# Kernel optimization log

Measured on AMD Instinct MI355X. Metric: run time of the kernel, lower is better.

## Reference

```python
import jax, jax.numpy as jnp
import numpy as np

N, C, CS, H = 2048, 768, 384, 16
D = C // H  # 48, per-head dim


def _ln(x, eps=1e-5):
    # torch LayerNorm: population variance over last dim
    m = jnp.mean(x, axis=-1, keepdims=True)
    v = jnp.var(x, axis=-1, keepdims=True)
    return (x - m) * jax.lax.rsqrt(v + eps)


def setup_inputs() -> dict:
    key = jax.random.key(0)
    ks = jax.random.split(key, 12)
    s = 0.02  # small init scale for weights
    return {
        "x": jax.random.normal(ks[0], (N, C), jnp.float32),
        "mask": jnp.ones((N,), jnp.float32),
        "pair_logits": jax.random.normal(ks[1], (H, N, N), jnp.float32),
        "single_cond": jax.random.normal(ks[2], (N, CS), jnp.float32),
        "q_w": jax.random.normal(ks[3], (C, C), jnp.float32) * s,
        "q_b": jnp.zeros((C,), jnp.float32),
        "k_w": jax.random.normal(ks[4], (C, C), jnp.float32) * s,
        "v_w": jax.random.normal(ks[5], (C, C), jnp.float32) * s,
        "gate_w": jax.random.normal(ks[6], (C, C), jnp.float32) * s,
        "sc_ln_w": jnp.ones((CS,), jnp.float32),
        "scale_w": jax.random.normal(ks[7], (C, CS), jnp.float32) * s,
        "scale_b": jnp.zeros((C,), jnp.float32),
        "bias_w": jax.random.normal(ks[8], (C, CS), jnp.float32) * s,
        "t2_w": jax.random.normal(ks[9], (C, C), jnp.float32) * s,
        "az_w": jax.random.normal(ks[10], (C, CS), jnp.float32) * s,
        "az_b": jnp.zeros((C,), jnp.float32),
    }


def reference(x, mask, pair_logits, single_cond, q_w, q_b, k_w, v_w, gate_w,
              sc_ln_w, scale_w, scale_b, bias_w, t2_w, az_w, az_b):
    n = x.shape[0]
    mask_bias = (1e9 * (mask - 1.0))[None, None, :]  # (1,1,N) additive bias
    # AdaptiveLayerNorm (use_single_cond=True)
    xn = _ln(x)                                      # no affine
    sc = _ln(single_cond) * sc_ln_w                  # LN with weight, no bias
    xm = jax.nn.sigmoid(sc @ scale_w.T + scale_b) * xn + sc @ bias_w.T
    # qkv projections -> (n, h, d)
    q = (xm @ q_w.T + q_b).reshape(n, H, D)
    k = (xm @ k_w.T).reshape(n, H, D)
    v = (xm @ v_w.T).reshape(n, H, D)
    logits = jnp.einsum('qhc,khc->hqk', q * (D ** -0.5), k) + mask_bias
    logits = logits + pair_logits
    weights = jax.nn.softmax(logits, axis=-1)        # (h, n, n)
    wavg = jnp.einsum('hqk,khc->qhc', weights, v).reshape(n, C)
    wavg = wavg * jax.nn.sigmoid(xm @ gate_w.T)      # sigmoid gating
    # AdaLNZero
    out = wavg @ t2_w.T
    out = jax.nn.sigmoid(single_cond @ az_w.T + az_b) * out
    return out
```

## Files before the change

kernel.cpp:

```cpp
#include <hip/hip_runtime.h>

typedef unsigned short u16;
typedef __attribute__((ext_vector_type(8))) short short8;
typedef __attribute__((ext_vector_type(4))) float f32x4;
typedef __attribute__((ext_vector_type(4))) unsigned short us4;

#define MFMA(a,b,c) __builtin_amdgcn_mfma_f32_16x16x32_bf16(a,b,c,0,0,0)
#define LOG2E 1.44269504088896341f
#define FENCE asm volatile("" ::: "memory")

__device__ __forceinline__ u16 f2bf(float f) {
  unsigned u = __builtin_bit_cast(unsigned, f);
  return (u16)((u + 0x7FFFu + ((u >> 16) & 1u)) >> 16);
}
__device__ __forceinline__ float bf2f(u16 u) {
  return __builtin_bit_cast(float, (unsigned)u << 16);
}
__device__ __forceinline__ unsigned cvtpk(float a, float b) {
  unsigned r;
  asm("v_cvt_pk_bf16_f32 %0, %1, %2" : "=v"(r) : "v"(a), "v"(b));
  return r;
}
__device__ __forceinline__ float sigmoidf_(float x) { return 1.f / (1.f + __expf(-x)); }

__device__ __forceinline__ void gload16(const void* g, void* l) {
  __builtin_amdgcn_global_load_lds(
      (const __attribute__((address_space(1))) void*)g,
      (__attribute__((address_space(3))) void*)l, 16, 0, 0);
}

__global__ __launch_bounds__(256) void cvt_weights(
    const float* __restrict__ sw, const float* __restrict__ bw, const float* __restrict__ aw,
    const float* __restrict__ qw, const float* __restrict__ kw, const float* __restrict__ vw,
    const float* __restrict__ gw, const float* __restrict__ tw,
    u16* __restrict__ wsb, u16* __restrict__ waz, u16* __restrict__ wqkvg, u16* __restrict__ wt2)
{
  long i = ((long)blockIdx.x * 256 + threadIdx.x) * 4;
  const float* src; u16* dst;
  if      (i < 294912)  { src = sw + i;             dst = wsb + i; }
  else if (i < 589824)  { src = bw + (i - 294912);  dst = wsb + i; }
  else if (i < 884736)  { src = aw + (i - 589824);  dst = waz + (i - 589824); }
  else if (i < 1474560) { src = qw + (i - 884736);  dst = wqkvg + (i - 884736); }
  else if (i < 2064384) { src = kw + (i - 1474560); dst = wqkvg + (i - 884736); }
  else if (i < 2654208) { src = vw + (i - 2064384); dst = wqkvg + (i - 884736); }
  else if (i < 3244032) { src = gw + (i - 2654208); dst = wqkvg + (i - 884736); }
  else                  { src = tw + (i - 3244032); dst = wt2 + (i - 3244032); }
  f32x4 v = *(const f32x4*)src;
  us4 o = { f2bf(v[0]), f2bf(v[1]), f2bf(v[2]), f2bf(v[3]) };
  *(us4*)dst = o;
}

__device__ __forceinline__ void blockreduce2(float& a, float& b) {
  #pragma unroll
  for (int d = 1; d < 64; d <<= 1) { a += __shfl_xor(a, d); b += __shfl_xor(b, d); }
  __shared__ float red[8];
  int w = threadIdx.x >> 6, l = threadIdx.x & 63;
  if (l == 0) { red[w] = a; red[4 + w] = b; }
  __syncthreads();
  a = red[0] + red[1] + red[2] + red[3];
  b = red[4] + red[5] + red[6] + red[7];
}

__global__ __launch_bounds__(256) void ln_prep(
    const float* __restrict__ x, const float* __restrict__ sc,
    const float* __restrict__ sc_ln_w, const float* __restrict__ mask,
    float* __restrict__ xn, u16* __restrict__ sc_bf, u16* __restrict__ scr_bf,
    float* __restrict__ mbv)
{
  int bid = blockIdx.x, t = threadIdx.x;
  if (bid < 2048) {
    const float* row = x + (long)bid * 768;
    float v0 = row[t], v1 = row[t + 256], v2 = row[t + 512];
    float s = v0 + v1 + v2, sq = v0*v0 + v1*v1 + v2*v2;
    blockreduce2(s, sq);
    float mean = s * (1.f / 768.f);
    float var = sq * (1.f / 768.f) - mean * mean;
    float rs = rsqrtf(var + 1e-5f);
    float* orow = xn + (long)bid * 768;
    orow[t] = (v0 - mean) * rs; orow[t + 256] = (v1 - mean) * rs; orow[t + 512] = (v2 - mean) * rs;
  } else if (bid < 4096) {
    int r = bid - 2048;
    const float* row = sc + (long)r * 384;
    float v0 = row[t];
    float v1 = (t < 128) ? row[t + 256] : 0.f;
    float s = v0 + v1, sq = v0*v0 + v1*v1;
    blockreduce2(s, sq);
    float mean = s * (1.f / 384.f), var = sq * (1.f / 384.f) - mean * mean;
    float rs = rsqrtf(var + 1e-5f);
    sc_bf[r*384 + t]  = f2bf((v0 - mean) * rs * sc_ln_w[t]);
    scr_bf[r*384 + t] = f2bf(v0);
    if (t < 128) {
      sc_bf[r*384 + t + 256]  = f2bf((v1 - mean) * rs * sc_ln_w[t + 256]);
      scr_bf[r*384 + t + 256] = f2bf(v1);
    }
  } else {
    for (int i = t; i < 2048; i += 256) mbv[i] = 1e9f * (mask[i] - 1.f);
  }
}

__global__ __launch_bounds__(256) void gemm_bf16_64(
    const u16* __restrict__ X, const u16* __restrict__ W,
    float* __restrict__ Y, int M, int K)
{
  __shared__ u16 lA[2048];
  __shared__ u16 lB[2048];
  const int row0 = blockIdx.x << 6;
  const int col0 = blockIdx.y << 6;
  const int tid = threadIdx.x;
  const int w = tid >> 6, l = tid & 63;
  const int wr = (w >> 1) << 5, wc = (w & 1) << 5;
  const int g = l >> 4, r16 = l & 15;
  const int srow = w * 16 + (l >> 2);
  const int scol = (l & 3) * 8;
  f32x4 acc[2][2] = {};
  for (int k0 = 0; k0 < K; k0 += 32) {
    gload16(X + (long)(row0 + srow) * K + k0 + scol, &lA[w*512]);
    gload16(W + (long)(col0 + srow) * K + k0 + scol, &lB[w*512]);
    __syncthreads();
    short8 af[2], bw_[2];
    #pragma unroll
    for (int i = 0; i < 2; ++i) { af[i]  = *(const short8*)&lA[(wr + i*16 + r16)*32 + g*8]; }
    #pragma unroll
    for (int j = 0; j < 2; ++j) { bw_[j] = *(const short8*)&lB[(wc + j*16 + r16)*32 + g*8]; }
    #pragma unroll
    for (int i = 0; i < 2; ++i)
      #pragma unroll
      for (int j = 0; j < 2; ++j)
        acc[i][j] = MFMA(af[i], bw_[j], acc[i][j]);
    __syncthreads();
  }
  #pragma unroll
  for (int i = 0; i < 2; ++i) {
    #pragma unroll
    for (int j = 0; j < 2; ++j) {
      long rr = row0 + wr + i*16 + g*4;
      int cc = col0 + wc + j*16 + r16;
      #pragma unroll
      for (int r = 0; r < 4; ++r) { Y[(rr + r) * M + cc] = acc[i][j][r]; }
    }
  }
}

__global__ __launch_bounds__(256) void gemm_az64(
    const u16* __restrict__ X, const u16* __restrict__ W,
    const float* __restrict__ azs, float* __restrict__ Y, int M, int K)
{
  __shared__ u16 lA[2048];
  __shared__ u16 lB[2048];
  const int row0 = blockIdx.x << 6;
  const int col0 = blockIdx.y << 6;
  const int tid = threadIdx.x;
  const int w = tid >> 6, l = tid & 63;
  const int wr = (w >> 1) << 5, wc = (w & 1) << 5;
  const int g = l >> 4, r16 = l & 15;
  const int srow = w * 16 + (l >> 2);
  const int scol = (l & 3) * 8;
  f32x4 acc[2][2] = {};
  for (int k0 = 0; k0 < K; k0 += 32) {
    gload16(X + (long)(row0 + srow) * K + k0 + scol, &lA[w*512]);
    gload16(W + (long)(col0 + srow) * K + k0 + scol, &lB[w*512]);
    __syncthreads();
    short8 af[2], bw_[2];
    #pragma unroll
    for (int i = 0; i < 2; ++i) { af[i]  = *(const short8*)&lA[(wr + i*16 + r16)*32 + g*8]; }
    #pragma unroll
    for (int j = 0; j < 2; ++j) { bw_[j] = *(const short8*)&lB[(wc + j*16 + r16)*32 + g*8]; }
    #pragma unroll
    for (int i = 0; i < 2; ++i)
      #pragma unroll
      for (int j = 0; j < 2; ++j)
        acc[i][j] = MFMA(af[i], bw_[j], acc[i][j]);
    __syncthreads();
  }
  #pragma unroll
  for (int i = 0; i < 2; ++i) {
    #pragma unroll
    for (int j = 0; j < 2; ++j) {
      long rr = row0 + wr + i*16 + g*4;
      int cc = col0 + wc + j*16 + r16;
      #pragma unroll
      for (int r = 0; r < 4; ++r) {
        Y[(rr + r) * M + cc] = acc[i][j][r] * azs[(rr + r) * M + cc];
      }
    }
  }
}

__global__ __launch_bounds__(256) void gemm_qkvg64(
    const u16* __restrict__ X, const u16* __restrict__ W,
    const float* __restrict__ q_b,
    u16* __restrict__ qpad, u16* __restrict__ kpad,
    u16* __restrict__ vt, u16* __restrict__ gsig)
{
  __shared__ u16 lA[2048];
  __shared__ u16 lB[2048];
  const int K = 768;
  const int row0 = blockIdx.x << 6;
  const int col0 = blockIdx.y << 6;
  const int tid = threadIdx.x;
  const int w = tid >> 6, l = tid & 63;
  const int wr = (w >> 1) << 5, wc = (w & 1) << 5;
  const int g = l >> 4, r16 = l & 15;
  const int srow = w * 16 + (l >> 2);
  const int scol = (l & 3) * 8;
  f32x4 acc[2][2] = {};
  for (int k0 = 0; k0 < K; k0 += 32) {
    gload16(X + (long)(row0 + srow) * K + k0 + scol, &lA[w*512]);
    gload16(W + (long)(col0 + srow) * K + k0 + scol, &lB[w*512]);
    __syncthreads();
    short8 af[2], bw_[2];
    #pragma unroll
    for (int i = 0; i < 2; ++i) { af[i]  = *(const short8*)&lA[(wr + i*16 + r16)*32 + g*8]; }
    #pragma unroll
    for (int j = 0; j < 2; ++j) { bw_[j] = *(const short8*)&lB[(wc + j*16 + r16)*32 + g*8]; }
    #pragma unroll
    for (int i = 0; i < 2; ++i)
      #pragma unroll
      for (int j = 0; j < 2; ++j)
        acc[i][j] = MFMA(af[i], bw_[j], acc[i][j]);
    __syncthreads();
  }
  const int sec = (col0 >= 2304) ? 3 : (col0 >= 1536) ? 2 : (col0 >= 768) ? 1 : 0;
  #pragma unroll
  for (int i = 0; i < 2; ++i) {
    #pragma unroll
    for (int j = 0; j < 2; ++j) {
      int rr = row0 + wr + i*16 + g*4;
      int cc = col0 + wc + j*16 + r16;
      if (sec == 0) {
        int m = cc, h = m / 48, d = m - h * 48;
        float qb = q_b[m];
        #pragma unroll
        for (int r = 0; r < 4; ++r)
          qpad[((long)h*2048 + rr + r)*64 + d] =
              f2bf((acc[i][j][r] + qb) * 0.14433756729740643f);
      } else if (sec == 1) {
        int m = cc - 768, h = m / 48, d = m - h * 48;
        #pragma unroll
        for (int r = 0; r < 4; ++r)
          kpad[((long)h*2048 + rr + r)*64 + d] = f2bf(acc[i][j][r]);
      } else if (sec == 2) {
        int m = cc - 1536, h = m / 48, d = m - h * 48;
        us4 o = { f2bf(acc[i][j][0]), f2bf(acc[i][j][1]),
                  f2bf(acc[i][j][2]), f2bf(acc[i][j][3]) };
        *(us4*)(vt + ((long)h*48 + d)*2048 + rr) = o;
      } else {
        int m = cc - 2304;
        #pragma unroll
        for (int r = 0; r < 4; ++r)
          gsig[(long)(rr + r)*768 + m] = f2bf(sigmoidf_(acc[i][j][r]));
      }
    }
  }
}

__global__ __launch_bounds__(256) void pad_init(
    const float* __restrict__ mbv, u16* __restrict__ qpad, u16* __restrict__ kpad)
{
  int t = blockIdx.x * 256 + threadIdx.x;
  int n = t & 2047;
  long base = (long)t * 64 + 48;
  us4 z = {0, 0, 0, 0};
  us4 q0 = { f2bf(1.0f), 0, 0, 0 };
  us4 k0 = { f2bf(mbv[n]), 0, 0, 0 };
  *(us4*)(qpad + base) = q0;  *(us4*)(qpad + base + 4) = z;
  *(us4*)(qpad + base + 8) = z; *(us4*)(qpad + base + 12) = z;
  *(us4*)(kpad + base) = k0;  *(us4*)(kpad + base + 4) = z;
  *(us4*)(kpad + base + 8) = z; *(us4*)(kpad + base + 12) = z;
}

__global__ __launch_bounds__(256) void ada_kernel(
    const float* __restrict__ Y1, const float* __restrict__ Yaz,
    const float* __restrict__ xn, const float* __restrict__ scale_b,
    const float* __restrict__ az_b, u16* __restrict__ xm, float* __restrict__ azsig)
{
  long e = ((long)blockIdx.x * 256 + threadIdx.x) * 4;
  int n = (int)(e / 768), c = (int)(e % 768);
  f32x4 ys = *(const f32x4*)(Y1 + (long)n*1536 + c);
  f32x4 yb = *(const f32x4*)(Y1 + (long)n*1536 + 768 + c);
  f32x4 xv = *(const f32x4*)(xn + e);
  f32x4 sb = *(const f32x4*)(scale_b + c);
  f32x4 ya = *(const f32x4*)(Yaz + e);
  f32x4 ab = *(const f32x4*)(az_b + c);
  us4 o; f32x4 az;
  #pragma unroll
  for (int k = 0; k < 4; ++k) {
    o[k] = f2bf(sigmoidf_(ys[k] + sb[k]) * xv[k] + yb[k]);
    az[k] = sigmoidf_(ya[k] + ab[k]);
  }
  *(us4*)(xm + e) = o;
  *(f32x4*)(azsig + e) = az;
}

__global__ __launch_bounds__(256, 3) void attn_kernel(
    const u16* __restrict__ qpad, const u16* __restrict__ kpad,
    const u16* __restrict__ vt, const float* __restrict__ pair,
    const u16* __restrict__ gsig, u16* __restrict__ wg)
{
  __shared__ __align__(16) char smem[36864];
  const int bid = blockIdx.x;
  const int h = ((bid & 7) << 1) | ((bid >> 3) & 1);
  const int qb = bid >> 4;
  const int tid = threadIdx.x, w = tid >> 6, l = tid & 63;
  const int g = l >> 4, q = l & 15;
  const int qrow = qb * 64 + w * 16 + q;

  const u16* qbase = qpad + ((long)h * 2048 + qrow) * 64;
  short8 qf0 = *(const short8*)(qbase + g * 8);
  short8 qf1 = *(const short8*)(qbase + 32 + g * 8);

  const float* prow = pair + ((long)h * 2048 + qrow) * 2048;
  const u16*   kgl  = kpad + (long)h * 2048 * 64;
  const u16*   vgl  = vt   + (long)h * 48 * 2048;
  const int sr8 = l >> 3, sc8 = l & 7;
  unsigned* pl = (unsigned*)(smem + 28672) + w*512 + q*32;
  const int sx = (q & 7) << 2;

  f32x4 prA[4], prB[4];

  #define STAGE_PR(KT, BUF) do {                                                  \
    _Pragma("unroll")                                                             \
    for (int mf_ = 0; mf_ < 4; ++mf_)                                             \
      BUF[mf_] = __builtin_nontemporal_load(                                      \
          (const f32x4*)(prow + (long)(KT)*64 + mf_*16 + g*4));                   \
  } while (0)

  #define STAGE_KV(KT, BI) do {                                                   \
    char* kd = smem + (BI)*8192 + w*2048;                                          \
    _Pragma("unroll")                                                              \
    for (int i_ = 0; i_ < 2; ++i_) {                                               \
      int row_ = i_*8 + sr8;                                                       \
      gload16(kgl + (long)((KT)*64 + w*16 + row_)*64 + ((sc8 ^ (row_&7)) << 3),    \
              kd + i_*1024);                                                       \
    }                                                                              \
    if (w > 0) {                                                                   \
      char* vd = smem + 16384 + (BI)*6144 + (w-1)*2048;                            \
      _Pragma("unroll")                                                            \
      for (int i_ = 0; i_ < 2; ++i_) {                                             \
        int row_ = i_*8 + sr8;                                                     \
        gload16(vgl + (long)((w-1)*16 + row_)*2048 + (KT)*64 +                     \
                ((sc8 ^ (row_&7)) << 3), vd + i_*1024);                            \
      }                                                                            \
    }                                                                              \
  } while (0)

  STAGE_PR(0, prA); STAGE_KV(0, 0);
  STAGE_PR(1, prB); STAGE_KV(1, 1);

  float m = -1e30f, ssum = 0.f;
  f32x4 o0 = {0,0,0,0}, o1 = {0,0,0,0}, o2 = {0,0,0,0};

  #define BODY(T, PRBUF, PAR) do {                                                \
    if ((T) == 31)   { asm volatile("s_waitcnt vmcnt(0)" ::: "memory"); }          \
    else if (w == 0) { asm volatile("s_waitcnt vmcnt(6)" ::: "memory"); }          \
    else             { asm volatile("s_waitcnt vmcnt(8)" ::: "memory"); }          \
    __builtin_amdgcn_s_barrier();                                                  \
    FENCE;                                                                         \
    const char* kb = smem + (PAR)*8192;                                            \
    const char* vb = smem + 16384 + (PAR)*6144;                                    \
    f32x4 s[4];                                                                    \
    _Pragma("unroll")                                                              \
    for (int mf = 0; mf < 4; ++mf) {                                               \
      const int kr = mf*16 + q;                                                    \
      short8 ka = *(const short8*)(kb + kr*128 + ((g       ^ (q&7)) << 4));        \
      short8 kc = *(const short8*)(kb + kr*128 + (((g + 4) ^ (q&7)) << 4));        \
      s[mf] = MFMA(ka, qf0, PRBUF[mf]);                                            \
      s[mf] = MFMA(kc, qf1, s[mf]);                                                \
    }                                                                              \
    float tmax = -3e38f;                                                           \
    _Pragma("unroll")                                                              \
    for (int mf = 0; mf < 4; ++mf)                                                 \
      tmax = fmaxf(tmax, fmaxf(fmaxf(s[mf][0], s[mf][1]), fmaxf(s[mf][2], s[mf][3])));\
    tmax = fmaxf(tmax, __shfl_xor(tmax, 16));                                      \
    tmax = fmaxf(tmax, __shfl_xor(tmax, 32));                                      \
    float mnew = fmaxf(m, tmax);                                                   \
    float alpha = exp2f((m - mnew) * LOG2E);                                       \
    m = mnew;                                                                      \
    float mL = mnew * LOG2E;                                                       \
    float psum = 0.f;                                                              \
    unsigned pk0[4], pk1[4];                                                       \
    _Pragma("unroll")                                                              \
    for (int mf = 0; mf < 4; ++mf) {                                               \
      float p0 = exp2f(fmaf(s[mf][0], LOG2E, -mL));                                \
      float p1 = exp2f(fmaf(s[mf][1], LOG2E, -mL));                                \
      float p2 = exp2f(fmaf(s[mf][2], LOG2E, -mL));                                \
      float p3 = exp2f(fmaf(s[mf][3], LOG2E, -mL));                                \
      psum += (p0 + p1) + (p2 + p3);                                               \
      pk0[mf] = cvtpk(p0, p1);                                                     \
      pk1[mf] = cvtpk(p2, p3);                                                     \
    }                                                                              \
    ssum = ssum * alpha + psum;                                                    \
    o0 *= alpha; o1 *= alpha; o2 *= alpha;                                         \
    _Pragma("unroll")                                                              \
    for (int mf = 0; mf < 4; ++mf) {                                               \
      uint2 pv_; pv_.x = pk0[mf]; pv_.y = pk1[mf];                                 \
      *(uint2*)(pl + ((mf*8 + g*2) ^ sx)) = pv_;                                   \
    }                                                                              \
    asm volatile("s_waitcnt lgkmcnt(0)" ::: "memory");                             \
    __builtin_amdgcn_sched_barrier(0);                                             \
    _Pragma("unroll")                                                              \
    for (int ks = 0; ks < 2; ++ks) {                                               \
      union { uint4 u4; short8 v; } pf;                                            \
      pf.u4 = *(const uint4*)(pl + ((ks*16 + g*4) ^ sx));                          \
      const int vc = ((ks*4 + g) ^ (q & 7)) << 4;                                  \
      short8 v0 = *(const short8*)(vb + (q)*128      + vc);                        \
      short8 v1 = *(const short8*)(vb + (16 + q)*128 + vc);                        \
      short8 v2 = *(const short8*)(vb + (32 + q)*128 + vc);                        \
      o0 = MFMA(v0, pf.v, o0);                                                     \
      o1 = MFMA(v1, pf.v, o1);                                                     \
      o2 = MFMA(v2, pf.v, o2);                                                     \
    }                                                                              \
    FENCE;                                                                         \
    __builtin_amdgcn_s_barrier();                                                  \
    FENCE;                                                                         \
    if ((T) < 30) { STAGE_PR((T)+2, PRBUF); STAGE_KV((T)+2, PAR); }                \
    __builtin_amdgcn_sched_barrier(0);                                             \
  } while (0)

  for (int t = 0; t < 32; t += 2) {
    BODY(t,     prA, 0);
    BODY(t + 1, prB, 1);
  }
  #undef BODY
  #undef STAGE_PR
  #undef STAGE_KV

  ssum += __shfl_xor(ssum, 16);
  ssum += __shfl_xor(ssum, 32);
  float rinv = 1.f / ssum;
  const long nbase = (long)qrow * 768 + h * 48;
  #pragma unroll
  for (int r = 0; r < 3; ++r) {
    f32x4 ov = (r == 0) ? o0 : ((r == 1) ? o1 : o2);
    int c = r * 16 + g * 4;
    us4 gs = *(const us4*)(gsig + nbase + c);
    us4 ou;
    #pragma unroll
    for (int j = 0; j < 4; ++j) ou[j] = f2bf(ov[j] * rinv * bf2f(gs[j]));
    *(us4*)(wg + nbase + c) = ou;
  }
}

extern "C" void kernel_launch(void* const* d_in, const int* in_sizes, int n_in,
                              void* d_out, int out_size, void* d_ws, size_t ws_size,
                              hipStream_t stream) {
  const float* x       = (const float*)d_in[0];
  const float* mask    = (const float*)d_in[1];
  const float* pair    = (const float*)d_in[2];
  const float* sc      = (const float*)d_in[3];
  const float* q_w     = (const float*)d_in[4];
  const float* q_b     = (const float*)d_in[5];
  const float* k_w     = (const float*)d_in[6];
  const float* v_w     = (const float*)d_in[7];
  const float* g_w     = (const float*)d_in[8];
  const float* slw     = (const float*)d_in[9];
  const float* scale_w = (const float*)d_in[10];
  const float* scale_b = (const float*)d_in[11];
  const float* bias_w  = (const float*)d_in[12];
  const float* t2_w    = (const float*)d_in[13];
  const float* az_w    = (const float*)d_in[14];
  const float* az_b    = (const float*)d_in[15];
  float* out = (float*)d_out;
  char* ws = (char*)d_ws;

  u16*   Wsb   = (u16*)  (ws + 0);
  u16*   Waz   = (u16*)  (ws + 1179648);
  u16*   Wqkvg = (u16*)  (ws + 1769472);
  u16*   Wt2   = (u16*)  (ws + 6488064);
  float* xn    = (float*)(ws + 7667712);
  u16*   sc_bf = (u16*)  (ws + 13959168);
  u16*   scr_bf= (u16*)  (ws + 15532032);
  u16*   wg    = (u16*)  (ws + 13959168);
  float* mb    = (float*)(ws + 17104896);
  float* Y1    = (float*)(ws + 17113088);
  u16*   qpad  = (u16*)  (ws + 17113088);
  u16*   kpad  = (u16*)  (ws + 21307392);
  float* Yaz   = (float*)(ws + 29696000);
  u16*   xm    = (u16*)  (ws + 35987456);
  float* azsig = (float*)(ws + 39133184);
  u16*   vt    = (u16*)  (ws + 70590464);
  u16*   gsig  = (u16*)  (ws + 73736192);

  cvt_weights<<<3744, 256, 0, stream>>>(scale_w, bias_w, az_w, q_w, k_w, v_w, g_w, t2_w,
                                        Wsb, Waz, Wqkvg, Wt2);
  ln_prep<<<4097, 256, 0, stream>>>(x, sc, slw, mask, xn, sc_bf, scr_bf, mb);
  gemm_bf16_64<<<dim3(32, 24), 256, 0, stream>>>(sc_bf, Wsb, Y1, 1536, 384);
  gemm_bf16_64<<<dim3(32, 12), 256, 0, stream>>>(scr_bf, Waz, Yaz, 768, 384);
  ada_kernel<<<1536, 256, 0, stream>>>(Y1, Yaz, xn, scale_b, az_b, xm, azsig);
  gemm_qkvg64<<<dim3(32, 48), 256, 0, stream>>>(xm, Wqkvg, q_b, qpad, kpad, vt, gsig);
  pad_init<<<128, 256, 0, stream>>>(mb, qpad, kpad);
  attn_kernel<<<512, 256, 0, stream>>>(qpad, kpad, vt, pair, gsig, wg);
  gemm_az64<<<dim3(32, 12), 256, 0, stream>>>(wg, Wt2, azsig, out, 768, 768);
}
```

Baseline: 164.0 us.

## Split attention over two key halves with a separate combine kernel

Splits the attention kernel along the key dimension into two halves (split-K / flash-decoding style). The grid doubles from 512 to 1024 blocks, and each block writes unnormalized partial outputs plus its running max and sum to workspace. A new combine kernel rescales the two partials, normalizes, applies the sigmoid gate and writes bf16 output. This targets low occupancy, since 512 blocks at 3 per CU underfill 256 CUs. The cost is extra fp32 partial traffic, one more launch, and a shorter pipelined loop per block.

```diff
diff --git a/kernel.cpp b/kernel.cpp
--- a/kernel.cpp
+++ b/kernel.cpp
@@ -292,15 +292,16 @@
   *(f32x4*)(azsig + e) = az;
 }
 
-__global__ __launch_bounds__(256, 3) void attn_kernel(
+__global__ __launch_bounds__(256, 3) void attn_partial(
     const u16* __restrict__ qpad, const u16* __restrict__ kpad,
     const u16* __restrict__ vt, const float* __restrict__ pair,
-    const u16* __restrict__ gsig, u16* __restrict__ wg)
+    float* __restrict__ po, float* __restrict__ pms)
 {
   __shared__ __align__(16) char smem[36864];
   const int bid = blockIdx.x;
   const int h = ((bid & 7) << 1) | ((bid >> 3) & 1);
-  const int qb = bid >> 4;
+  const int kh = (bid >> 4) & 1;
+  const int qb = bid >> 5;
   const int tid = threadIdx.x, w = tid >> 6, l = tid & 63;
   const int g = l >> 4, q = l & 15;
   const int qrow = qb * 64 + w * 16 + q;
@@ -309,9 +310,9 @@
   short8 qf0 = *(const short8*)(qbase + g * 8);
   short8 qf1 = *(const short8*)(qbase + 32 + g * 8);
 
-  const float* prow = pair + ((long)h * 2048 + qrow) * 2048;
-  const u16*   kgl  = kpad + (long)h * 2048 * 64;
-  const u16*   vgl  = vt   + (long)h * 48 * 2048;
+  const float* prow = pair + ((long)h * 2048 + qrow) * 2048 + kh * 1024;
+  const u16*   kgl  = kpad + (long)h * 2048 * 64 + (long)kh * 1024 * 64;
+  const u16*   vgl  = vt   + (long)h * 48 * 2048 + kh * 1024;
   const int sr8 = l >> 3, sc8 = l & 7;
   unsigned* pl = (unsigned*)(smem + 28672) + w*512 + q*32;
   const int sx = (q & 7) << 2;
@@ -351,7 +352,7 @@
   f32x4 o0 = {0,0,0,0}, o1 = {0,0,0,0}, o2 = {0,0,0,0};
 
   #define BODY(T, PRBUF, PAR) do {                                                \
-    if ((T) == 31)   { asm volatile("s_waitcnt vmcnt(0)" ::: "memory"); }          \
+    if ((T) == 15)   { asm volatile("s_waitcnt vmcnt(0)" ::: "memory"); }          \
     else if (w == 0) { asm volatile("s_waitcnt vmcnt(6)" ::: "memory"); }          \
     else             { asm volatile("s_waitcnt vmcnt(8)" ::: "memory"); }          \
     __builtin_amdgcn_s_barrier();                                                  \
@@ -413,11 +414,11 @@
     FENCE;                                                                         \
     __builtin_amdgcn_s_barrier();                                                  \
     FENCE;                                                                         \
-    if ((T) < 30) { STAGE_PR((T)+2, PRBUF); STAGE_KV((T)+2, PAR); }                \
+    if ((T) < 14) { STAGE_PR((T)+2, PRBUF); STAGE_KV((T)+2, PAR); }                \
     __builtin_amdgcn_sched_barrier(0);                                             \
   } while (0)
 
-  for (int t = 0; t < 32; t += 2) {
+  for (int t = 0; t < 16; t += 2) {
     BODY(t,     prA, 0);
     BODY(t + 1, prB, 1);
   }
@@ -427,18 +428,35 @@
 
   ssum += __shfl_xor(ssum, 16);
   ssum += __shfl_xor(ssum, 32);
-  float rinv = 1.f / ssum;
-  const long nbase = (long)qrow * 768 + h * 48;
+  if (g == 0) {
+    *(float2*)(pms + ((long)(kh*16 + h)*2048 + qrow)*2) = make_float2(m, ssum);
+  }
+  const long pbase = (long)kh*1572864 + (long)qrow*768 + h*48;
+  *(f32x4*)(po + pbase + g*4)      = o0;
+  *(f32x4*)(po + pbase + 16 + g*4) = o1;
+  *(f32x4*)(po + pbase + 32 + g*4) = o2;
+}
+
+__global__ __launch_bounds__(256) void attn_combine(
+    const float* __restrict__ po, const float* __restrict__ pms,
+    const u16* __restrict__ gsig, u16* __restrict__ wg)
+{
+  long e = ((long)blockIdx.x * 256 + threadIdx.x) * 4;
+  int n = (int)(e / 768), c = (int)(e % 768), h = c / 48;
+  f32x4 a0 = *(const f32x4*)(po + e);
+  f32x4 a1 = *(const f32x4*)(po + 1572864 + e);
+  float2 p0 = *(const float2*)(pms + ((long)h*2048 + n)*2);
+  float2 p1 = *(const float2*)(pms + ((long)(16+h)*2048 + n)*2);
+  float M = fmaxf(p0.x, p1.x);
+  float e0 = exp2f((p0.x - M) * LOG2E);
+  float e1 = exp2f((p1.x - M) * LOG2E);
+  float rinv = 1.f / (p0.y * e0 + p1.y * e1);
+  us4 gs = *(const us4*)(gsig + e);
+  us4 ou;
   #pragma unroll
-  for (int r = 0; r < 3; ++r) {
-    f32x4 ov = (r == 0) ? o0 : ((r == 1) ? o1 : o2);
-    int c = r * 16 + g * 4;
-    us4 gs = *(const us4*)(gsig + nbase + c);
-    us4 ou;
-    #pragma unroll
-    for (int j = 0; j < 4; ++j) ou[j] = f2bf(ov[j] * rinv * bf2f(gs[j]));
-    *(us4*)(wg + nbase + c) = ou;
-  }
+  for (int j = 0; j < 4; ++j)
+    ou[j] = f2bf((a0[j]*e0 + a1[j]*e1) * rinv * bf2f(gs[j]));
+  *(us4*)(wg + e) = ou;
 }
 
 extern "C" void kernel_launch(void* const* d_in, const int* in_sizes, int n_in,
@@ -478,6 +496,8 @@
   float* Yaz   = (float*)(ws + 29696000);
   u16*   xm    = (u16*)  (ws + 35987456);
   float* azsig = (float*)(ws + 39133184);
+  float* po    = (float*)(ws + 45424640);
+  float* pms   = (float*)(ws + 58007552);
   u16*   vt    = (u16*)  (ws + 70590464);
   u16*   gsig  = (u16*)  (ws + 73736192);
 
@@ -489,6 +509,7 @@
   ada_kernel<<<1536, 256, 0, stream>>>(Y1, Yaz, xn, scale_b, az_b, xm, azsig);
   gemm_qkvg64<<<dim3(32, 48), 256, 0, stream>>>(xm, Wqkvg, q_b, qpad, kpad, vt, gsig);
   pad_init<<<128, 256, 0, stream>>>(mb, qpad, kpad);
-  attn_kernel<<<512, 256, 0, stream>>>(qpad, kpad, vt, pair, gsig, wg);
+  attn_partial<<<1024, 256, 0, stream>>>(qpad, kpad, vt, pair, po, pms);
+  attn_combine<<<1536, 256, 0, stream>>>(po, pms, gsig, wg);
   gemm_az64<<<dim3(32, 12), 256, 0, stream>>>(wg, Wt2, azsig, out, 768, 768);
 }
```

After: 173.6 us. +5.8%, slower.
